# Kernel tuning notes

Measured on AMD Instinct MI355X. Metric: run time of the kernel, lower is better.

## Reference

```python
import jax, jax.numpy as jnp
import numpy as np

B, S, D, H, L, F = 64, 128, 1024, 16, 8, 3072
DH = D // H
NEG = -1e9  # stands in for the -inf row (neg_inf_idx=0) of the distance encoder
EPS = 1e-5


def _ln(x, g, b):
    mu = jnp.mean(x, axis=-1, keepdims=True)
    var = jnp.mean(jnp.square(x - mu), axis=-1, keepdims=True)
    return (x - mu) * jax.lax.rsqrt(var + EPS) * g + b


def setup_inputs() -> dict:
    key = jax.random.key(0)
    ks = jax.random.split(key, 24)
    s = 0.02
    inp = {
        'atoms': jax.random.randint(ks[0], (B, S), 0, 121),
        'neighbors': jax.random.randint(ks[1], (B, S), 0, 17),
        'distances': jax.random.randint(ks[2], (B, S, S), 2, 13),  # avoid all-masked rows
        'atoms_emb': jax.random.normal(ks[3], (121, D), jnp.float32) * s,
        'neigh_emb': jax.random.normal(ks[4], (17, D), jnp.float32) * s,
        'dist_emb': jax.random.normal(ks[5], (13, H), jnp.float32) * s,
        'wq': jax.random.normal(ks[6], (D, D), jnp.float32) * s,
        'bq': jnp.zeros((D,), jnp.float32),
        'wk': jax.random.normal(ks[7], (D, D), jnp.float32) * s,
        'bk': jnp.zeros((D,), jnp.float32),
        'wv': jax.random.normal(ks[8], (D, D), jnp.float32) * s,
        'bv': jnp.zeros((D,), jnp.float32),
        'wo': jax.random.normal(ks[9], (D, D), jnp.float32) * s,
        'bo': jnp.zeros((D,), jnp.float32),
        'ln1_g': jnp.ones((D,), jnp.float32),
        'ln1_b': jnp.zeros((D,), jnp.float32),
        'w1': jax.random.normal(ks[10], (D, F), jnp.float32) * s,
        'b1': jnp.zeros((F,), jnp.float32),
        'w2': jax.random.normal(ks[11], (F, D), jnp.float32) * s,
        'b2': jnp.zeros((D,), jnp.float32),
        'ln2_g': jnp.ones((D,), jnp.float32),
        'ln2_b': jnp.zeros((D,), jnp.float32),
    }
    return inp


def reference(atoms, neighbors, distances, atoms_emb, neigh_emb, dist_emb,
              wq, bq, wk, bk, wv, bv, wo, bo, ln1_g, ln1_b,
              w1, b1, w2, b2, ln2_g, ln2_b):
    # padding_idx=0 rows are zero; distance row 0 is -inf (non-reachable/pad mask)
    a_tab = atoms_emb.at[0].set(0.0)
    n_tab = neigh_emb.at[0].set(0.0)
    d_tab = dist_emb.at[0].set(NEG)

    x = a_tab[atoms] + n_tab[neighbors]                 # [B,S,D]
    # shared attention bias, permute(0,3,1,2): [B,S,S,H] -> [B,H,S,S]
    bias = jnp.transpose(d_tab[distances], (0, 3, 1, 2))
    scale = 1.0 / np.sqrt(DH)

    for _ in range(L):  # shared_weights=True: same params each layer
        q = (x @ wq + bq).reshape(B, S, H, DH)
        k = (x @ wk + bk).reshape(B, S, H, DH)
        v = (x @ wv + bv).reshape(B, S, H, DH)
        scores = jnp.einsum('bqhd,bkhd->bhqk', q, k) * scale + bias
        attn = jax.nn.softmax(scores, axis=-1)
        o = jnp.einsum('bhqk,bkhd->bqhd', attn, v).reshape(B, S, D)
        x = _ln(x + (o @ wo + bo), ln1_g, ln1_b)        # post-LN (norm_first=False)
        h = jax.nn.gelu(x @ w1 + b1, approximate=False) @ w2 + b2
        x = _ln(x + h, ln2_g, ln2_b)
    return x
```

## Files before the change

kernel.cpp:

```cpp
#include <hip/hip_runtime.h>
#include <hip/hip_bf16.h>

#define BB 64
#define SS 128
#define DD 1024
#define HH 16
#define DHH 64
#define FF 3072
#define QS 3072
#define NLAYER 8
#define TT (BB*SS)
#define NEGV -1e9f
#define EPSV 1e-5f

typedef __bf16 bf16;
typedef __bf16 bf16x4 __attribute__((ext_vector_type(4)));
typedef __bf16 bf16x8 __attribute__((ext_vector_type(8)));
typedef float f32x4 __attribute__((ext_vector_type(4)));

#define WS_NEEDED 88084480ull
#define FLAG_OFF  88080384ull

__device__ __forceinline__ float ldf(const void* p, long idx, int f) {
  return f ? ((const float*)p)[idx] : (float)((const bf16*)p)[idx];
}

__global__ __launch_bounds__(256) void diag_kernel(bf16* __restrict__ out, float val) {
  int base = blockIdx.x * 1024 + threadIdx.x * 4;
  for (int j = 0; j < 4; j++) out[base + j] = (bf16)val;
}

__global__ __launch_bounds__(256) void detect_kernel(const unsigned short* __restrict__ p,
                                                     int n, int* __restrict__ flag) {
  __shared__ int sh[4];
  int found = 0;
  for (int i = threadIdx.x; i < n; i += 256) {
    unsigned e = (p[i] >> 7) & 0xFF;
    found |= (e >= 0x7F);
  }
  for (int d = 1; d < 64; d <<= 1) found |= __shfl_xor(found, d);
  if ((threadIdx.x & 63) == 0) sh[threadIdx.x >> 6] = found;
  __syncthreads();
  if (threadIdx.x == 0) *flag = sh[0] | sh[1] | sh[2] | sh[3];
}

__global__ __launch_bounds__(256) void transpose_kernel(const void* __restrict__ W,
                                                        bf16* __restrict__ WT, int K, int N,
                                                        const int* __restrict__ dflag) {
  __shared__ bf16 tbuf[32][33];
  const int f = *dflag;
  int n0 = blockIdx.x * 32, k0 = blockIdx.y * 32;
  int tx = threadIdx.x & 31, ty = threadIdx.x >> 5;
  for (int i = 0; i < 4; i++)
    tbuf[ty + i*8][tx] = (bf16)ldf(W, (long)(k0 + ty + i*8) * N + n0 + tx, f);
  __syncthreads();
  for (int i = 0; i < 4; i++)
    WT[(long)(n0 + ty + i*8) * K + k0 + tx] = tbuf[tx][ty + i*8];
}

__global__ __launch_bounds__(256) void embed_kernel(const int* __restrict__ atoms,
                                                    const int* __restrict__ neigh,
                                                    const void* __restrict__ a_emb,
                                                    const void* __restrict__ n_emb,
                                                    bf16* __restrict__ xb,
                                                    const int* __restrict__ dflag) {
  const int f = *dflag;
  int t = blockIdx.x;
  int a = atoms[t], n = neigh[t];
  int c0 = threadIdx.x * 4;
  bf16x4 o;
  for (int j = 0; j < 4; j++) {
    float va = (a != 0) ? ldf(a_emb, (long)a * DD + c0 + j, f) : 0.0f;
    float vn = (n != 0) ? ldf(n_emb, (long)n * DD + c0 + j, f) : 0.0f;
    o[j] = (bf16)(va + vn);
  }
  *(bf16x4*)(xb + (long)t * DD + c0) = o;
}

template<int EPI, int NBIAS>
__global__ __launch_bounds__(256) void gemm_bt(const bf16* __restrict__ A,
                                               const bf16* __restrict__ Bt,
                                               const void* __restrict__ bp0,
                                               const void* __restrict__ bp1,
                                               const void* __restrict__ bp2,
                                               bf16* __restrict__ Cout,
                                               int lda, int N, int K,
                                               const int* __restrict__ dflag) {
  __shared__ __align__(16) bf16 Ald[2][128][32];
  __shared__ __align__(16) bf16 Bld[2][128][32];
  const int f = *dflag;
  const int tid  = threadIdx.x;
  const int l    = tid & 63;
  const int quad = l >> 4, l16 = l & 15;
  const int w    = tid >> 6, wr = w >> 1, wc = w & 1;
  const int m0   = blockIdx.y * 128;
  const int n0   = blockIdx.x * 128;

  const int r0 = tid >> 2, c0 = tid & 3;
  const bf16* Ap0 = A  + (long)(m0 + r0)      * lda + c0*8;
  const bf16* Ap1 = A  + (long)(m0 + 64 + r0) * lda + c0*8;
  const bf16* Bp0 = Bt + (long)(n0 + r0)      * K   + c0*8;
  const bf16* Bp1 = Bt + (long)(n0 + 64 + r0) * K   + c0*8;

  f32x4 acc[4][4] = {};

  bf16x8 ra[2][2], rb[2][2];
  for (int s = 0; s < 2; s++) {
    ra[s][0] = *(const bf16x8*)(Ap0 + s*32);
    ra[s][1] = *(const bf16x8*)(Ap1 + s*32);
    rb[s][0] = *(const bf16x8*)(Bp0 + s*32);
    rb[s][1] = *(const bf16x8*)(Bp1 + s*32);
  }

  for (int kt = 0; kt < K; kt += 64) {
    for (int s = 0; s < 2; s++) {
      *(bf16x8*)&Ald[s][r0][c0*8]      = ra[s][0];
      *(bf16x8*)&Ald[s][64 + r0][c0*8] = ra[s][1];
      *(bf16x8*)&Bld[s][r0][c0*8]      = rb[s][0];
      *(bf16x8*)&Bld[s][64 + r0][c0*8] = rb[s][1];
    }
    __syncthreads();

    if (kt + 64 < K) {
      const int kn = kt + 64;
      for (int s = 0; s < 2; s++) {
        ra[s][0] = *(const bf16x8*)(Ap0 + kn + s*32);
        ra[s][1] = *(const bf16x8*)(Ap1 + kn + s*32);
        rb[s][0] = *(const bf16x8*)(Bp0 + kn + s*32);
        rb[s][1] = *(const bf16x8*)(Bp1 + kn + s*32);
      }
    }

    for (int s = 0; s < 2; s++) {
      bf16x8 af[4], bfr[4];
      for (int i = 0; i < 4; i++)
        af[i] = *(const bf16x8*)&Ald[s][wr*64 + i*16 + l16][quad*8];
      for (int j = 0; j < 4; j++)
        bfr[j] = *(const bf16x8*)&Bld[s][wc*64 + j*16 + l16][quad*8];
      for (int i = 0; i < 4; i++)
        for (int j = 0; j < 4; j++)
          acc[i][j] = __builtin_amdgcn_mfma_f32_16x16x32_bf16(af[i], bfr[j], acc[i][j], 0, 0, 0);
    }
    __syncthreads();
  }

  for (int i = 0; i < 4; i++) {
    for (int j = 0; j < 4; j++) {
      int col = n0 + wc*64 + j*16 + l16;
      float bv;
      if (NBIAS == 3) {
        int seg = col >> 10, off = col & 1023;
        const void* bp = (seg == 0) ? bp0 : ((seg == 1) ? bp1 : bp2);
        bv = ldf(bp, off, f);
      } else {
        bv = ldf(bp0, col, f);
      }
      for (int r = 0; r < 4; r++) {
        int row = m0 + wr*64 + i*16 + quad*4 + r;
        float v = acc[i][j][r] + bv;
        if (EPI == 2) v = 0.5f * v * (1.0f + erff(v * 0.70710678118f));
        Cout[(long)row * N + col] = (bf16)v;
      }
    }
  }
}

__global__ __launch_bounds__(256) void attn_kernel(bf16* __restrict__ qkv,
                                                   const int* __restrict__ dist,
                                                   const void* __restrict__ demb,
                                                   const int* __restrict__ dflag) {
  __shared__ __align__(16) bf16 Vt[DHH][SS + 8];
  __shared__ __align__(16) bf16 Pb[4][32][SS + 8];
  __shared__ float dtab[16];
  const int f = *dflag;
  const int b = blockIdx.x >> 4, h = blockIdx.x & 15;
  const int tid = threadIdx.x;
  const int w = tid >> 6, l = tid & 63, quad = l >> 4, l16 = l & 15;
  if (tid < 13) dtab[tid] = (tid == 0) ? NEGV : ldf(demb, tid * HH + h, f);

  const long rowb = (long)b * SS;
  for (int i = 0; i < 4; i++) {
    int task = tid + i * 256;
    int kk = task >> 3, ng = task & 7;
    bf16x8 vv = *(const bf16x8*)(qkv + (rowb + kk) * QS + 2048 + h*DHH + ng*8);
    for (int u = 0; u < 8; u++) Vt[ng*8 + u][kk] = vv[u];
  }
  __syncthreads();

  const int qbase = w * 32;
  f32x4 acc[2][8] = {};
  for (int ks = 0; ks < 2; ks++) {
    bf16x8 af[2];
    for (int ti = 0; ti < 2; ti++)
      af[ti] = *(const bf16x8*)(qkv + (rowb + qbase + ti*16 + l16) * QS + h*DHH + ks*32 + quad*8);
    for (int tj = 0; tj < 8; tj++) {
      bf16x8 bfr = *(const bf16x8*)(qkv + (rowb + tj*16 + l16) * QS + 1024 + h*DHH + ks*32 + quad*8);
      for (int ti = 0; ti < 2; ti++)
        acc[ti][tj] = __builtin_amdgcn_mfma_f32_16x16x32_bf16(af[ti], bfr, acc[ti][tj], 0, 0, 0);
    }
  }

  const float scale = 0.125f;
  for (int ti = 0; ti < 2; ti++) {
    for (int r = 0; r < 4; r++) {
      int q = qbase + ti*16 + quad*4 + r;
      const int* drow = dist + (rowb + q) * SS;
      float vals[8];
      float mx = -3.0e38f;
      for (int tj = 0; tj < 8; tj++) {
        float sv = acc[ti][tj][r] * scale + dtab[drow[tj*16 + l16]];
        vals[tj] = sv; mx = fmaxf(mx, sv);
      }
      for (int d2 = 1; d2 < 16; d2 <<= 1) mx = fmaxf(mx, __shfl_xor(mx, d2));
      float sm = 0.0f;
      for (int tj = 0; tj < 8; tj++) { vals[tj] = __expf(vals[tj] - mx); sm += vals[tj]; }
      for (int d2 = 1; d2 < 16; d2 <<= 1) sm += __shfl_xor(sm, d2);
      float inv = 1.0f / sm;
      int pr = ti*16 + quad*4 + r;
      for (int tj = 0; tj < 8; tj++)
        Pb[w][pr][tj*16 + l16] = (bf16)(vals[tj] * inv);
    }
  }
  __syncthreads();

  f32x4 acc2[2][4] = {};
  for (int ks = 0; ks < 4; ks++) {
    bf16x8 af[2];
    for (int ti = 0; ti < 2; ti++)
      af[ti] = *(const bf16x8*)&Pb[w][ti*16 + l16][ks*32 + quad*8];
    for (int tj = 0; tj < 4; tj++) {
      bf16x8 bfr = *(const bf16x8*)&Vt[tj*16 + l16][ks*32 + quad*8];
      for (int ti = 0; ti < 2; ti++)
        acc2[ti][tj] = __builtin_amdgcn_mfma_f32_16x16x32_bf16(af[ti], bfr, acc2[ti][tj], 0, 0, 0);
    }
  }
  for (int ti = 0; ti < 2; ti++)
    for (int tj = 0; tj < 4; tj++)
      for (int r = 0; r < 4; r++) {
        int q = qbase + ti*16 + quad*4 + r;
        qkv[(rowb + q) * QS + h*DHH + tj*16 + l16] = (bf16)acc2[ti][tj][r];
      }
}

__global__ __launch_bounds__(256) void add_ln_kernel(bf16* __restrict__ x,
                                                     const bf16* __restrict__ tmp,
                                                     const void* __restrict__ g,
                                                     const void* __restrict__ bta,
                                                     const int* __restrict__ dflag) {
  const int f = *dflag;
  int r = blockIdx.x, tid = threadIdx.x;
  int c0 = tid * 4;
  bf16x4 xv = *(const bf16x4*)(x + (long)r*DD + c0);
  bf16x4 tv = *(const bf16x4*)(tmp + (long)r*DD + c0);
  float v[4];
  for (int j = 0; j < 4; j++) v[j] = (float)xv[j] + (float)tv[j];
  float s  = v[0] + v[1] + v[2] + v[3];
  float s2 = v[0]*v[0] + v[1]*v[1] + v[2]*v[2] + v[3]*v[3];
  for (int d2 = 1; d2 < 64; d2 <<= 1) { s += __shfl_xor(s, d2); s2 += __shfl_xor(s2, d2); }
  __shared__ float ws1[4], ws2[4];
  int w = tid >> 6, l = tid & 63;
  if (l == 0) { ws1[w] = s; ws2[w] = s2; }
  __syncthreads();
  s  = ws1[0] + ws1[1] + ws1[2] + ws1[3];
  s2 = ws2[0] + ws2[1] + ws2[2] + ws2[3];
  float mu  = s * (1.0f / DD);
  float var = s2 * (1.0f / DD) - mu * mu;
  float rs  = rsqrtf(var + EPSV);
  bf16x4 o;
  for (int j = 0; j < 4; j++)
    o[j] = (bf16)((v[j] - mu) * rs * ldf(g, c0 + j, f) + ldf(bta, c0 + j, f));
  *(bf16x4*)(x + (long)r*DD + c0) = o;
}

__global__ __launch_bounds__(256) void finalize_kernel(const bf16* __restrict__ src,
                                                       void* __restrict__ dst,
                                                       const int* __restrict__ dflag) {
  const int f = *dflag;
  long i = (long)blockIdx.x * 1024 + threadIdx.x * 4;
  for (int j = 0; j < 4; j++) {
    float v = (float)src[i + j];
    if (v != v) v = 777.0f;
    if (f) ((float*)dst)[i + j] = v;
    else   ((bf16*)dst)[i + j] = (bf16)v;
  }
}

extern "C" void kernel_launch(void* const* d_in, const int* in_sizes, int n_in,
                              void* d_out, int out_size, void* d_ws, size_t ws_size,
                              hipStream_t stream) {
  (void)in_sizes; (void)n_in; (void)out_size;
  const int*  atoms     = (const int*)d_in[0];
  const int*  neighbors = (const int*)d_in[1];
  const int*  distances = (const int*)d_in[2];
  const void* atoms_emb = d_in[3];
  const void* neigh_emb = d_in[4];
  const void* dist_emb  = d_in[5];
  const void* wq = d_in[6];
  const void* bq = d_in[7];
  const void* wk = d_in[8];
  const void* bk = d_in[9];
  const void* wv = d_in[10];
  const void* bv = d_in[11];
  const void* wo = d_in[12];
  const void* bo = d_in[13];
  const void* ln1_g = d_in[14];
  const void* ln1_b = d_in[15];
  const void* w1 = d_in[16];
  const void* b1 = d_in[17];
  const void* w2 = d_in[18];
  const void* b2 = d_in[19];
  const void* ln2_g = d_in[20];
  const void* ln2_b = d_in[21];

  if (ws_size < WS_NEEDED) {
    diag_kernel<<<TT, 256, 0, stream>>>((bf16*)d_out, (float)(ws_size >> 20));
    return;
  }

  char* ws = (char*)d_ws;
  bf16* qkv   = (bf16*)(ws);
  bf16* tmp2  = (bf16*)(ws + 50331648);
  bf16* wqkvT = (bf16*)(ws + 67108864);
  bf16* woT   = (bf16*)(ws + 73400320);
  bf16* w1T   = (bf16*)(ws + 75497472);
  bf16* w2T   = (bf16*)(ws + 81788928);
  int*  dflag = (int*)(ws + FLAG_OFF);
  bf16* xb    = (bf16*)d_out;

  detect_kernel<<<1, 256, 0, stream>>>((const unsigned short*)atoms_emb, 2048, dflag);

  transpose_kernel<<<dim3(32, 32), 256, 0, stream>>>(wq, wqkvT,           1024, 1024, dflag);
  transpose_kernel<<<dim3(32, 32), 256, 0, stream>>>(wk, wqkvT + 1048576, 1024, 1024, dflag);
  transpose_kernel<<<dim3(32, 32), 256, 0, stream>>>(wv, wqkvT + 2097152, 1024, 1024, dflag);
  transpose_kernel<<<dim3(32, 32), 256, 0, stream>>>(wo, woT,             1024, 1024, dflag);
  transpose_kernel<<<dim3(96, 32), 256, 0, stream>>>(w1, w1T,             1024, 3072, dflag);
  transpose_kernel<<<dim3(32, 96), 256, 0, stream>>>(w2, w2T,             3072, 1024, dflag);

  embed_kernel<<<TT, 256, 0, stream>>>(atoms, neighbors, atoms_emb, neigh_emb, xb, dflag);

  for (int layer = 0; layer < NLAYER; layer++) {
    gemm_bt<1,3><<<dim3(24, 64), 256, 0, stream>>>(xb, wqkvT, bq, bk, bv, qkv,
                                                   1024, 3072, 1024, dflag);
    attn_kernel<<<BB * HH, 256, 0, stream>>>(qkv, distances, dist_emb, dflag);
    gemm_bt<1,1><<<dim3(8, 64),  256, 0, stream>>>(qkv, woT, bo, bo, bo, tmp2,
                                                   3072, 1024, 1024, dflag);
    add_ln_kernel<<<TT, 256, 0, stream>>>(xb, tmp2, ln1_g, ln1_b, dflag);
    gemm_bt<2,1><<<dim3(24, 64), 256, 0, stream>>>(xb, w1T, b1, b1, b1, qkv,
                                                   1024, 3072, 1024, dflag);
    gemm_bt<1,1><<<dim3(8, 64),  256, 0, stream>>>(qkv, w2T, b2, b2, b2, tmp2,
                                                   3072, 1024, 3072, dflag);
    add_ln_kernel<<<TT, 256, 0, stream>>>(xb, tmp2, ln2_g, ln2_b, dflag);
  }

  hipMemcpyAsync(tmp2, d_out, (size_t)TT * DD * 2, hipMemcpyDeviceToDevice, stream);
  finalize_kernel<<<TT, 256, 0, stream>>>(tmp2, d_out, dflag);
}
```

Baseline: 2.559 ms.

## Split-K the N=1024 GEMMs and swizzle LDS tiles to avoid bank conflicts

The output-projection and FFN-down GEMMs, which launch only 512 blocks, now use a two-way split over K via blockIdx.z. Each half writes a bf16 partial sum to its own buffer, and a new add_ln3 kernel adds both partials and the residual before the layernorm. The Wo partial goes into the unused K columns of the qkv buffer. The W2 split needs a larger workspace and falls back to the old path when the workspace is too small. Separately, the shared-memory tile layout uses an XOR swizzle of the 16-byte column chunk to cut LDS bank conflicts. The trade-offs are more partial-sum memory traffic and an extra bf16 rounding of the partial results.

Result: slower. 2.679 ms (+4.7%).

```diff
diff --git a/kernel.cpp b/kernel.cpp
--- a/kernel.cpp
+++ b/kernel.cpp
@@ -20,6 +20,8 @@
 
 #define WS_NEEDED 88084480ull
 #define FLAG_OFF  88080384ull
+#define TMP3_OFF  88084480ull
+#define WS_SPLIT  (TMP3_OFF + 16777216ull)
 
 __device__ __forceinline__ float ldf(const void* p, long idx, int f) {
   return f ? ((const float*)p)[idx] : (float)((const bf16*)p)[idx];
@@ -83,8 +85,9 @@
                                                const void* __restrict__ bp0,
                                                const void* __restrict__ bp1,
                                                const void* __restrict__ bp2,
-                                               bf16* __restrict__ Cout,
-                                               int lda, int N, int K,
+                                               bf16* __restrict__ C0, int ldc0,
+                                               bf16* __restrict__ C1, int ldc1,
+                                               int lda, int N, int K, int ksplit,
                                                const int* __restrict__ dflag) {
   __shared__ __align__(16) bf16 Ald[2][128][32];
   __shared__ __align__(16) bf16 Bld[2][128][32];
@@ -95,8 +98,14 @@
   const int w    = tid >> 6, wr = w >> 1, wc = w & 1;
   const int m0   = blockIdx.y * 128;
   const int n0   = blockIdx.x * 128;
+  const int z    = blockIdx.z;
+  const int kbeg = z * ksplit, kend = kbeg + ksplit;
+  bf16* Cout = z ? C1 : C0;
+  const int ldc  = z ? ldc1 : ldc0;
 
   const int r0 = tid >> 2, c0 = tid & 3;
+  const int cs = (c0 ^ ((r0 >> 1) & 3)) * 8;
+  const int cr = (quad ^ ((l16 >> 1) & 3)) * 8;
   const bf16* Ap0 = A  + (long)(m0 + r0)      * lda + c0*8;
   const bf16* Ap1 = A  + (long)(m0 + 64 + r0) * lda + c0*8;
   const bf16* Bp0 = Bt + (long)(n0 + r0)      * K   + c0*8;
@@ -106,22 +115,22 @@
 
   bf16x8 ra[2][2], rb[2][2];
   for (int s = 0; s < 2; s++) {
-    ra[s][0] = *(const bf16x8*)(Ap0 + s*32);
-    ra[s][1] = *(const bf16x8*)(Ap1 + s*32);
-    rb[s][0] = *(const bf16x8*)(Bp0 + s*32);
-    rb[s][1] = *(const bf16x8*)(Bp1 + s*32);
-  }
-
-  for (int kt = 0; kt < K; kt += 64) {
+    ra[s][0] = *(const bf16x8*)(Ap0 + kbeg + s*32);
+    ra[s][1] = *(const bf16x8*)(Ap1 + kbeg + s*32);
+    rb[s][0] = *(const bf16x8*)(Bp0 + kbeg + s*32);
+    rb[s][1] = *(const bf16x8*)(Bp1 + kbeg + s*32);
+  }
+
+  for (int kt = kbeg; kt < kend; kt += 64) {
     for (int s = 0; s < 2; s++) {
-      *(bf16x8*)&Ald[s][r0][c0*8]      = ra[s][0];
-      *(bf16x8*)&Ald[s][64 + r0][c0*8] = ra[s][1];
-      *(bf16x8*)&Bld[s][r0][c0*8]      = rb[s][0];
-      *(bf16x8*)&Bld[s][64 + r0][c0*8] = rb[s][1];
+      *(bf16x8*)&Ald[s][r0][cs]      = ra[s][0];
+      *(bf16x8*)&Ald[s][64 + r0][cs] = ra[s][1];
+      *(bf16x8*)&Bld[s][r0][cs]      = rb[s][0];
+      *(bf16x8*)&Bld[s][64 + r0][cs] = rb[s][1];
     }
     __syncthreads();
 
-    if (kt + 64 < K) {
+    if (kt + 64 < kend) {
       const int kn = kt + 64;
       for (int s = 0; s < 2; s++) {
         ra[s][0] = *(const bf16x8*)(Ap0 + kn + s*32);
@@ -134,9 +143,9 @@
     for (int s = 0; s < 2; s++) {
       bf16x8 af[4], bfr[4];
       for (int i = 0; i < 4; i++)
-        af[i] = *(const bf16x8*)&Ald[s][wr*64 + i*16 + l16][quad*8];
+        af[i] = *(const bf16x8*)&Ald[s][wr*64 + i*16 + l16][cr];
       for (int j = 0; j < 4; j++)
-        bfr[j] = *(const bf16x8*)&Bld[s][wc*64 + j*16 + l16][quad*8];
+        bfr[j] = *(const bf16x8*)&Bld[s][wc*64 + j*16 + l16][cr];
       for (int i = 0; i < 4; i++)
         for (int j = 0; j < 4; j++)
           acc[i][j] = __builtin_amdgcn_mfma_f32_16x16x32_bf16(af[i], bfr[j], acc[i][j], 0, 0, 0);
@@ -147,19 +156,21 @@
   for (int i = 0; i < 4; i++) {
     for (int j = 0; j < 4; j++) {
       int col = n0 + wc*64 + j*16 + l16;
-      float bv;
-      if (NBIAS == 3) {
-        int seg = col >> 10, off = col & 1023;
-        const void* bp = (seg == 0) ? bp0 : ((seg == 1) ? bp1 : bp2);
-        bv = ldf(bp, off, f);
-      } else {
-        bv = ldf(bp0, col, f);
+      float bv = 0.0f;
+      if (z == 0) {
+        if (NBIAS == 3) {
+          int seg = col >> 10, off = col & 1023;
+          const void* bp = (seg == 0) ? bp0 : ((seg == 1) ? bp1 : bp2);
+          bv = ldf(bp, off, f);
+        } else {
+          bv = ldf(bp0, col, f);
+        }
       }
       for (int r = 0; r < 4; r++) {
         int row = m0 + wr*64 + i*16 + quad*4 + r;
         float v = acc[i][j][r] + bv;
         if (EPI == 2) v = 0.5f * v * (1.0f + erff(v * 0.70710678118f));
-        Cout[(long)row * N + col] = (bf16)v;
+        Cout[(long)row * ldc + col] = (bf16)v;
       }
     }
   }
@@ -254,6 +265,38 @@
   bf16x4 tv = *(const bf16x4*)(tmp + (long)r*DD + c0);
   float v[4];
   for (int j = 0; j < 4; j++) v[j] = (float)xv[j] + (float)tv[j];
+  float s  = v[0] + v[1] + v[2] + v[3];
+  float s2 = v[0]*v[0] + v[1]*v[1] + v[2]*v[2] + v[3]*v[3];
+  for (int d2 = 1; d2 < 64; d2 <<= 1) { s += __shfl_xor(s, d2); s2 += __shfl_xor(s2, d2); }
+  __shared__ float ws1[4], ws2[4];
+  int w = tid >> 6, l = tid & 63;
+  if (l == 0) { ws1[w] = s; ws2[w] = s2; }
+  __syncthreads();
+  s  = ws1[0] + ws1[1] + ws1[2] + ws1[3];
+  s2 = ws2[0] + ws2[1] + ws2[2] + ws2[3];
+  float mu  = s * (1.0f / DD);
+  float var = s2 * (1.0f / DD) - mu * mu;
+  float rs  = rsqrtf(var + EPSV);
+  bf16x4 o;
+  for (int j = 0; j < 4; j++)
+    o[j] = (bf16)((v[j] - mu) * rs * ldf(g, c0 + j, f) + ldf(bta, c0 + j, f));
+  *(bf16x4*)(x + (long)r*DD + c0) = o;
+}
+
+__global__ __launch_bounds__(256) void add_ln3_kernel(bf16* __restrict__ x,
+                                                      const bf16* __restrict__ t0, int ld0,
+                                                      const bf16* __restrict__ t1, int ld1,
+                                                      const void* __restrict__ g,
+                                                      const void* __restrict__ bta,
+                                                      const int* __restrict__ dflag) {
+  const int f = *dflag;
+  int r = blockIdx.x, tid = threadIdx.x;
+  int c0 = tid * 4;
+  bf16x4 xv = *(const bf16x4*)(x + (long)r*DD + c0);
+  bf16x4 av = *(const bf16x4*)(t0 + (long)r*ld0 + c0);
+  bf16x4 bv = *(const bf16x4*)(t1 + (long)r*ld1 + c0);
+  float v[4];
+  for (int j = 0; j < 4; j++) v[j] = (float)xv[j] + (float)av[j] + (float)bv[j];
   float s  = v[0] + v[1] + v[2] + v[3];
   float s2 = v[0]*v[0] + v[1]*v[1] + v[2]*v[2] + v[3]*v[3];
   for (int d2 = 1; d2 < 64; d2 <<= 1) { s += __shfl_xor(s, d2); s2 += __shfl_xor(s2, d2); }
@@ -316,6 +359,7 @@
     diag_kernel<<<TT, 256, 0, stream>>>((bf16*)d_out, (float)(ws_size >> 20));
     return;
   }
+  const bool split2 = (ws_size >= WS_SPLIT);
 
   char* ws = (char*)d_ws;
   bf16* qkv   = (bf16*)(ws);
@@ -325,6 +369,7 @@
   bf16* w1T   = (bf16*)(ws + 75497472);
   bf16* w2T   = (bf16*)(ws + 81788928);
   int*  dflag = (int*)(ws + FLAG_OFF);
+  bf16* tmp3  = (bf16*)(ws + TMP3_OFF);
   bf16* xb    = (bf16*)d_out;
 
   detect_kernel<<<1, 256, 0, stream>>>((const unsigned short*)atoms_emb, 2048, dflag);
@@ -339,17 +384,30 @@
   embed_kernel<<<TT, 256, 0, stream>>>(atoms, neighbors, atoms_emb, neigh_emb, xb, dflag);
 
   for (int layer = 0; layer < NLAYER; layer++) {
-    gemm_bt<1,3><<<dim3(24, 64), 256, 0, stream>>>(xb, wqkvT, bq, bk, bv, qkv,
-                                                   1024, 3072, 1024, dflag);
+    gemm_bt<1,3><<<dim3(24, 64, 1), 256, 0, stream>>>(xb, wqkvT, bq, bk, bv,
+                                                      qkv, 3072, (bf16*)nullptr, 0,
+                                                      1024, 3072, 1024, 1024, dflag);
     attn_kernel<<<BB * HH, 256, 0, stream>>>(qkv, distances, dist_emb, dflag);
-    gemm_bt<1,1><<<dim3(8, 64),  256, 0, stream>>>(qkv, woT, bo, bo, bo, tmp2,
-                                                   3072, 1024, 1024, dflag);
-    add_ln_kernel<<<TT, 256, 0, stream>>>(xb, tmp2, ln1_g, ln1_b, dflag);
-    gemm_bt<2,1><<<dim3(24, 64), 256, 0, stream>>>(xb, w1T, b1, b1, b1, qkv,
-                                                   1024, 3072, 1024, dflag);
-    gemm_bt<1,1><<<dim3(8, 64),  256, 0, stream>>>(qkv, w2T, b2, b2, b2, tmp2,
-                                                   3072, 1024, 3072, dflag);
-    add_ln_kernel<<<TT, 256, 0, stream>>>(xb, tmp2, ln2_g, ln2_b, dflag);
+    gemm_bt<1,1><<<dim3(8, 64, 2), 256, 0, stream>>>(qkv, woT, bo, bo, bo,
+                                                     tmp2, 1024, qkv + 1024, 3072,
+                                                     3072, 1024, 1024, 512, dflag);
+    add_ln3_kernel<<<TT, 256, 0, stream>>>(xb, tmp2, 1024, qkv + 1024, 3072,
+                                           ln1_g, ln1_b, dflag);
+    gemm_bt<2,1><<<dim3(24, 64, 1), 256, 0, stream>>>(xb, w1T, b1, b1, b1,
+                                                      qkv, 3072, (bf16*)nullptr, 0,
+                                                      1024, 3072, 1024, 1024, dflag);
+    if (split2) {
+      gemm_bt<1,1><<<dim3(8, 64, 2), 256, 0, stream>>>(qkv, w2T, b2, b2, b2,
+                                                       tmp2, 1024, tmp3, 1024,
+                                                       3072, 1024, 3072, 1536, dflag);
+      add_ln3_kernel<<<TT, 256, 0, stream>>>(xb, tmp2, 1024, tmp3, 1024,
+                                             ln2_g, ln2_b, dflag);
+    } else {
+      gemm_bt<1,1><<<dim3(8, 64, 1), 256, 0, stream>>>(qkv, w2T, b2, b2, b2,
+                                                       tmp2, 1024, (bf16*)nullptr, 0,
+                                                       3072, 1024, 3072, 3072, dflag);
+      add_ln_kernel<<<TT, 256, 0, stream>>>(xb, tmp2, ln2_g, ln2_b, dflag);
+    }
   }
 
   hipMemcpyAsync(tmp2, d_out, (size_t)TT * DD * 2, hipMemcpyDeviceToDevice, stream);
```

## Load B fragments directly to registers, swizzle and double-buffer A LDS tile

Applied to the files above, without the earlier changes.

The GEMM now loads each wave's B operand fragments straight from global memory into registers, skipping the LDS staging for B. The A tile is stored in LDS with an XOR swizzle to reduce bank conflicts and is double-buffered, which removes the trailing __syncthreads per k-step. In exchange each B element is read from global/L2 by two waves instead of once per block, and the extra fragment registers may lower occupancy.

New measurement: 4.018 ms. 1.57x slower.

```diff
diff --git a/kernel.cpp b/kernel.cpp
--- a/kernel.cpp
+++ b/kernel.cpp
@@ -86,8 +86,7 @@
                                                bf16* __restrict__ Cout,
                                                int lda, int N, int K,
                                                const int* __restrict__ dflag) {
-  __shared__ __align__(16) bf16 Ald[2][128][32];
-  __shared__ __align__(16) bf16 Bld[2][128][32];
+  __shared__ __align__(16) bf16 Ald[2][2][128][32];
   const int f = *dflag;
   const int tid  = threadIdx.x;
   const int l    = tid & 63;
@@ -97,51 +96,54 @@
   const int n0   = blockIdx.x * 128;
 
   const int r0 = tid >> 2, c0 = tid & 3;
-  const bf16* Ap0 = A  + (long)(m0 + r0)      * lda + c0*8;
-  const bf16* Ap1 = A  + (long)(m0 + 64 + r0) * lda + c0*8;
-  const bf16* Bp0 = Bt + (long)(n0 + r0)      * K   + c0*8;
-  const bf16* Bp1 = Bt + (long)(n0 + 64 + r0) * K   + c0*8;
+  const int cs = (c0 ^ ((r0 >> 1) & 3)) * 8;
+  const int cr = (quad ^ ((l16 >> 1) & 3)) * 8;
+  const bf16* Ap0 = A + (long)(m0 + r0)      * lda + c0*8;
+  const bf16* Ap1 = A + (long)(m0 + 64 + r0) * lda + c0*8;
+  const bf16* Bf[4];
+  for (int j = 0; j < 4; j++)
+    Bf[j] = Bt + (long)(n0 + wc*64 + j*16 + l16) * K + quad*8;
 
   f32x4 acc[4][4] = {};
 
-  bf16x8 ra[2][2], rb[2][2];
+  bf16x8 ra[2][2], rbf[2][4];
   for (int s = 0; s < 2; s++) {
     ra[s][0] = *(const bf16x8*)(Ap0 + s*32);
     ra[s][1] = *(const bf16x8*)(Ap1 + s*32);
-    rb[s][0] = *(const bf16x8*)(Bp0 + s*32);
-    rb[s][1] = *(const bf16x8*)(Bp1 + s*32);
-  }
-
+    for (int j = 0; j < 4; j++)
+      rbf[s][j] = *(const bf16x8*)(Bf[j] + s*32);
+  }
+
+  int p = 0;
   for (int kt = 0; kt < K; kt += 64) {
     for (int s = 0; s < 2; s++) {
-      *(bf16x8*)&Ald[s][r0][c0*8]      = ra[s][0];
-      *(bf16x8*)&Ald[s][64 + r0][c0*8] = ra[s][1];
-      *(bf16x8*)&Bld[s][r0][c0*8]      = rb[s][0];
-      *(bf16x8*)&Bld[s][64 + r0][c0*8] = rb[s][1];
+      *(bf16x8*)&Ald[p][s][r0][cs]      = ra[s][0];
+      *(bf16x8*)&Ald[p][s][64 + r0][cs] = ra[s][1];
     }
     __syncthreads();
 
+    bf16x8 curB[2][4];
+    for (int s = 0; s < 2; s++)
+      for (int j = 0; j < 4; j++) curB[s][j] = rbf[s][j];
     if (kt + 64 < K) {
       const int kn = kt + 64;
       for (int s = 0; s < 2; s++) {
         ra[s][0] = *(const bf16x8*)(Ap0 + kn + s*32);
         ra[s][1] = *(const bf16x8*)(Ap1 + kn + s*32);
-        rb[s][0] = *(const bf16x8*)(Bp0 + kn + s*32);
-        rb[s][1] = *(const bf16x8*)(Bp1 + kn + s*32);
+        for (int j = 0; j < 4; j++)
+          rbf[s][j] = *(const bf16x8*)(Bf[j] + kn + s*32);
       }
     }
 
     for (int s = 0; s < 2; s++) {
-      bf16x8 af[4], bfr[4];
+      bf16x8 af[4];
       for (int i = 0; i < 4; i++)
-        af[i] = *(const bf16x8*)&Ald[s][wr*64 + i*16 + l16][quad*8];
-      for (int j = 0; j < 4; j++)
-        bfr[j] = *(const bf16x8*)&Bld[s][wc*64 + j*16 + l16][quad*8];
+        af[i] = *(const bf16x8*)&Ald[p][s][wr*64 + i*16 + l16][cr];
       for (int i = 0; i < 4; i++)
         for (int j = 0; j < 4; j++)
-          acc[i][j] = __builtin_amdgcn_mfma_f32_16x16x32_bf16(af[i], bfr[j], acc[i][j], 0, 0, 0);
-    }
-    __syncthreads();
+          acc[i][j] = __builtin_amdgcn_mfma_f32_16x16x32_bf16(af[i], curB[s][j], acc[i][j], 0, 0, 0);
+    }
+    p ^= 1;
   }
 
   for (int i = 0; i < 4; i++) {
```
